# Optimization experiments

Hardware: AMD Instinct MI355X
Metric: run time of the kernel (lower is better)

The kernel has to match this reference:

```python
import jax, jax.numpy as jnp
import numpy as np

W0 = 30.0  # Sine frequency


def _bilinear_sample(plane, gx, gy):
    """torch.grid_sample(mode='bilinear', padding_mode='zeros', align_corners=True).
    plane: (C,H,W); gx,gy: (P,) normalized coords in [-1,1]. Returns (P,C)."""
    C, H, W = plane.shape
    ix = (gx + 1.0) * 0.5 * (W - 1)
    iy = (gy + 1.0) * 0.5 * (H - 1)
    x0 = jnp.floor(ix); y0 = jnp.floor(iy)
    x1 = x0 + 1.0;      y1 = y0 + 1.0
    wx1 = ix - x0; wx0 = 1.0 - wx1
    wy1 = iy - y0; wy0 = 1.0 - wy1

    def corner(xc, yc, w):
        valid = ((xc >= 0) & (xc <= W - 1) & (yc >= 0) & (yc <= H - 1)).astype(plane.dtype)
        xi = jnp.clip(xc, 0, W - 1).astype(jnp.int32)
        yi = jnp.clip(yc, 0, H - 1).astype(jnp.int32)
        return plane[:, yi, xi] * (w * valid)  # (C,P)

    out = (corner(x0, y0, wx0 * wy0) + corner(x1, y0, wx1 * wy0)
           + corner(x0, y1, wx0 * wy1) + corner(x1, y1, wx1 * wy1))
    return out.T  # (P,C)


def setup_inputs() -> dict:
    key = jax.random.key(0)
    ks = jax.random.split(key, 8)
    N = 500_000
    C, H, W = 128, 256, 256
    coords = jax.random.uniform(ks[0], (1, N, 3), jnp.float32, minval=-1.0, maxval=1.0)
    planes = [jax.random.normal(ks[1 + i], (1, C, H, W), jnp.float32) * 0.1 for i in range(3)]
    # Linear weights: first layer sine init, then frequency_init(30) for layers 2,3
    W1 = jax.random.uniform(ks[4], (C, C), jnp.float32, minval=-1.0 / C, maxval=1.0 / C)
    lim = np.sqrt(6.0 / C) / W0
    W2 = jax.random.uniform(ks[5], (C, C), jnp.float32, minval=-lim, maxval=lim)
    W3 = jax.random.uniform(ks[6], (1, C), jnp.float32, minval=-lim, maxval=lim)
    return {
        "coordinates": coords,
        "plane_xy": planes[0], "plane_yz": planes[1], "plane_xz": planes[2],
        "W1": W1, "b1": jnp.zeros((C,), jnp.float32),
        "W2": W2, "b2": jnp.zeros((C,), jnp.float32),
        "W3": W3, "b3": jnp.zeros((1,), jnp.float32),
    }


def reference(coordinates, plane_xy, plane_yz, plane_xz, W1, b1, W2, b2, W3, b3):
    B, N, _ = coordinates.shape  # B must be 1 (plane batch is 1, as in torch)
    c = coordinates.reshape(-1, 3)
    p0 = plane_xy[0]
    # NOTE: original module samples the *xz* coords from embeddings[0] (plane_xy) —
    # a bug we faithfully preserve — and multiplies [xy, xz, xz]; yz_embed is unused.
    xy = _bilinear_sample(p0, c[:, 0], c[:, 1])  # (P,C)
    xz = _bilinear_sample(p0, c[:, 0], c[:, 2])  # (P,C)
    features = xy * xz * xz
    h = jnp.sin(W0 * (features @ W1.T + b1))
    h = jnp.sin(W0 * (h @ W2.T + b2))
    out = h @ W3.T + b3
    return out.reshape(B, N, 1)
```

## Files before the change

kernel.cpp:

```cpp
#include <hip/hip_runtime.h>
#include <hip/hip_fp16.h>

typedef float f32x4 __attribute__((ext_vector_type(4)));
typedef _Float16 f16x8 __attribute__((ext_vector_type(8)));

#define CDIM 128
#define HW 256
#define NBINS 256
#define BINCAP 2560
#define TILES_PER_BIN 10
#define BINS_PER_XCD 32
#define GRID_MAIN 256

#define LDS_FENCE() asm volatile("" ::: "memory")

__global__ __launch_bounds__(256) void k_transpose(const float* __restrict__ plane,
                                                   unsigned short* __restrict__ planeT) {
    __shared__ unsigned short tile[32][130];
    int tid = threadIdx.x;
    int y  = blockIdx.x >> 3;
    int x0 = (blockIdx.x & 7) * 32;
    int tx = tid & 31, tc = tid >> 5;
    for (int cc = 0; cc < 128; cc += 8) {
        int c = cc + tc;
        float v = plane[c * (HW * HW) + y * HW + x0 + tx];
        tile[tx][c] = __half_as_ushort(__float2half(v));
    }
    __syncthreads();
    for (int it = 0; it < 16; ++it) {
        int idx = it * 256 + tid;
        int c = idx & 127, xi = idx >> 7;
        planeT[(y * HW + x0 + xi) * CDIM + c] = tile[xi][c];
    }
}

__global__ __launch_bounds__(256) void k_wconv(const float* __restrict__ W1,
                                               const float* __restrict__ W2,
                                               unsigned short* __restrict__ W1h,
                                               unsigned short* __restrict__ W2h) {
    int i = blockIdx.x * 256 + threadIdx.x;
    if (i < 16384) W1h[i] = __half_as_ushort(__float2half(W1[i]));
    else           W2h[i - 16384] = __half_as_ushort(__float2half(W2[i - 16384]));
}

__global__ __launch_bounds__(256) void k_scatter(const float* __restrict__ coords,
                                                 float4* __restrict__ bins,
                                                 int* __restrict__ cursor, int N) {
    __shared__ int hist[NBINS];
    __shared__ int rnk[NBINS];
    __shared__ int base[NBINS];
    const int tid = threadIdx.x;
    hist[tid] = 0; rnk[tid] = 0;
    __syncthreads();

    const int start = blockIdx.x * 2048;
    float gx[8], gy[8], gz[8]; int bn[8];
#pragma unroll
    for (int k = 0; k < 8; ++k) {
        int p = start + k * 256 + tid;
        if (p < N) {
            gx[k] = coords[p * 3 + 0];
            gy[k] = coords[p * 3 + 1];
            gz[k] = coords[p * 3 + 2];
            float ix = (gx[k] + 1.f) * 127.5f;
            bn[k] = max(0, min((int)floorf(ix), HW - 1));
            atomicAdd(&hist[bn[k]], 1);
        } else bn[k] = -1;
    }
    __syncthreads();
    if (hist[tid] > 0) base[tid] = atomicAdd(&cursor[tid], hist[tid]);
    __syncthreads();
#pragma unroll
    for (int k = 0; k < 8; ++k) {
        if (bn[k] >= 0) {
            int p = start + k * 256 + tid;
            int r = atomicAdd(&rnk[bn[k]], 1);
            int pos = base[bn[k]] + r;
            if (pos < BINCAP) {
                float4 rec; rec.x = gx[k]; rec.y = gy[k]; rec.z = gz[k];
                rec.w = __int_as_float(p);
                bins[(size_t)bn[k] * BINCAP + pos] = rec;
            }
        }
    }
}

struct PrepT {
    int off[8];
    __half2 w[4];
    __half2 v[4];
};

__device__ __forceinline__ PrepT prepV(float gx, float gy, float gz, int cg) {
    PrepT r;
    float ix = (gx + 1.f) * 127.5f;
    float iy = (gy + 1.f) * 127.5f;
    float iz = (gz + 1.f) * 127.5f;
    float xf = floorf(ix), yf = floorf(iy), zf = floorf(iz);
    float wx1 = ix - xf, wy1 = iy - yf, wz1 = iz - zf;
    float wx0 = 1.f - wx1, wy0 = 1.f - wy1, wz0 = 1.f - wz1;
    int x0 = max(0, min((int)xf, HW - 1));
    int y0 = max(0, min((int)yf, HW - 1));
    int z0 = max(0, min((int)zf, HW - 1));
    int x1 = min(x0 + 1, HW - 1);
    int y1 = min(y0 + 1, HW - 1);
    int z1 = min(z0 + 1, HW - 1);
    int cx0 = x0 * CDIM + cg * 8, cx1 = x1 * CDIM + cg * 8;
    r.off[0] = (y0 << 15) + cx0; r.off[1] = (y0 << 15) + cx1;
    r.off[2] = (y1 << 15) + cx0; r.off[3] = (y1 << 15) + cx1;
    r.off[4] = (z0 << 15) + cx0; r.off[5] = (z0 << 15) + cx1;
    r.off[6] = (z1 << 15) + cx0; r.off[7] = (z1 << 15) + cx1;
    r.w[0] = __float2half2_rn(wy0 * wx0);
    r.w[1] = __float2half2_rn(wy0 * wx1);
    r.w[2] = __float2half2_rn(wy1 * wx0);
    r.w[3] = __float2half2_rn(wy1 * wx1);
    r.v[0] = __float2half2_rn(wz0 * wx0);
    r.v[1] = __float2half2_rn(wz0 * wx1);
    r.v[2] = __float2half2_rn(wz1 * wx0);
    r.v[3] = __float2half2_rn(wz1 * wx1);
    return r;
}

struct LdT { uint4 d[8]; };

__device__ __forceinline__ LdT ld8(const unsigned short* __restrict__ planeT, const PrepT& a) {
    LdT r;
#pragma unroll
    for (int c = 0; c < 8; ++c)
        r.d[c] = *reinterpret_cast<const uint4*>(planeT + a.off[c]);
    return r;
}

__device__ __forceinline__ __half2 geth2(const uint4& u, int g) {
    const unsigned* p = reinterpret_cast<const unsigned*>(&u);
    return __builtin_bit_cast(__half2, p[g]);
}

__device__ __forceinline__ void interp_store(unsigned short* dst, const PrepT& a, const LdT& L) {
    unsigned o[4];
#pragma unroll
    for (int g = 0; g < 4; ++g) {
        __half2 xy = __hmul2(a.w[0], geth2(L.d[0], g));
        xy = __hfma2(a.w[1], geth2(L.d[1], g), xy);
        xy = __hfma2(a.w[2], geth2(L.d[2], g), xy);
        xy = __hfma2(a.w[3], geth2(L.d[3], g), xy);
        __half2 xz = __hmul2(a.v[0], geth2(L.d[4], g));
        xz = __hfma2(a.v[1], geth2(L.d[5], g), xz);
        xz = __hfma2(a.v[2], geth2(L.d[6], g), xz);
        xz = __hfma2(a.v[3], geth2(L.d[7], g), xz);
        __half2 f = __hmul2(xy, __hmul2(xz, xz));
        o[g] = __builtin_bit_cast(unsigned, f);
    }
    uint4 pack; pack.x = o[0]; pack.y = o[1]; pack.z = o[2]; pack.w = o[3];
    *reinterpret_cast<uint4*>(dst) = pack;
}

template <bool SORTED>
__global__ __launch_bounds__(512, 2) void k_all(const float* __restrict__ coords,
                                                const float4* __restrict__ bins,
                                                const int* __restrict__ cursor,
                                                const unsigned short* __restrict__ planeT,
                                                const unsigned short* __restrict__ W1h,
                                                const unsigned short* __restrict__ W2h,
                                                const float* __restrict__ b1,
                                                const float* __restrict__ b2,
                                                const float* __restrict__ W3,
                                                const float* __restrict__ b3,
                                                float* __restrict__ out, int N) {
    __shared__ alignas(16) uint4 W1L[128][16];
    __shared__ alignas(16) uint4 W2L[128][16];
    __shared__ alignas(16) unsigned short featS[256][128];

    const int tid  = threadIdx.x;
    const int wave = tid >> 6, lane = tid & 63;
    const int ro2  = wave * 32;
    const int j = lane & 15, rg = lane >> 4;
    const int pt = lane >> 4, cg = lane & 15;

#pragma unroll
    for (int i = 0; i < 4; ++i) {
        int idx = i * 512 + tid;
        int row = idx >> 4, col = idx & 15;
        W1L[row][col ^ (row & 15)] = reinterpret_cast<const uint4*>(W1h)[idx];
        W2L[row][col ^ (row & 15)] = reinterpret_cast<const uint4*>(W2h)[idx];
    }
    float b1v[8], b2v[8], w3v[8];
#pragma unroll
    for (int nt = 0; nt < 8; ++nt) {
        b1v[nt] = 30.f * b1[nt * 16 + j];
        b2v[nt] = 30.f * b2[nt * 16 + j];
        w3v[nt] = W3[nt * 16 + j];
    }
    const float bb3 = b3[0];
    __syncthreads();

    const int ntt = SORTED ? (NBINS * TILES_PER_BIN) : ((N + 255) >> 8);
    for (int tt = blockIdx.x; tt < ntt; tt += gridDim.x) {
        int bin = 0, base = 0, cnt = 0, pbase = 0;
        if (SORTED) {
            int xcd = tt & 7, jj = tt >> 3;
            bin  = xcd * BINS_PER_XCD + jj / TILES_PER_BIN;
            base = (jj % TILES_PER_BIN) * 256;
            cnt  = min(cursor[bin], BINCAP);
            if (base >= cnt) continue;
        } else {
            pbase = tt * 256 + ro2;
        }
        const float4* brec = bins + (size_t)bin * BINCAP;

#pragma unroll
        for (int grp = 0; grp < 2; ++grp) {
            PrepT a0, a1, a2, a3;
#pragma unroll
            for (int it = 0; it < 4; ++it) {
                int pl = grp * 16 + it * 4 + pt;
                float gx, gy, gz;
                if (SORTED) {
                    int q = min(base + ro2 + pl, cnt - 1);
                    float4 s = brec[q];
                    gx = s.x; gy = s.y; gz = s.z;
                } else {
                    int p = min(pbase + pl, N - 1);
                    gx = coords[p * 3 + 0];
                    gy = coords[p * 3 + 1];
                    gz = coords[p * 3 + 2];
                }
                PrepT a = prepV(gx, gy, gz, cg);
                if (it == 0) a0 = a; else if (it == 1) a1 = a;
                else if (it == 2) a2 = a; else a3 = a;
            }
            LdT d0 = ld8(planeT, a0);
            LdT d1 = ld8(planeT, a1);
            LdT d2 = ld8(planeT, a2);
            LdT d3 = ld8(planeT, a3);
            int r0 = grp * 16 + 0 * 4 + pt;
            int r1 = grp * 16 + 1 * 4 + pt;
            int r2 = grp * 16 + 2 * 4 + pt;
            int r3 = grp * 16 + 3 * 4 + pt;
            interp_store(&featS[ro2 + r0][(cg ^ (r0 & 15)) * 8], a0, d0);
            interp_store(&featS[ro2 + r1][(cg ^ (r1 & 15)) * 8], a1, d1);
            interp_store(&featS[ro2 + r2][(cg ^ (r2 & 15)) * 8], a2, d2);
            interp_store(&featS[ro2 + r3][(cg ^ (r3 & 15)) * 8], a3, d3);
        }

        LDS_FENCE();

        f32x4 acc[2][8];
#pragma unroll
        for (int g = 0; g < 2; ++g)
#pragma unroll
            for (int nt = 0; nt < 8; ++nt) acc[g][nt] = (f32x4){0.f, 0.f, 0.f, 0.f};

        f16x8 af[2][4];
#pragma unroll
        for (int g = 0; g < 2; ++g)
#pragma unroll
            for (int kk = 0; kk < 4; ++kk)
                af[g][kk] = __builtin_bit_cast(f16x8, *reinterpret_cast<const uint4*>(
                    &featS[ro2 + g * 16 + j][((kk * 4 + rg) ^ j) * 8]));

#pragma unroll
        for (int kk = 0; kk < 4; ++kk) {
            f16x8 bf[8];
#pragma unroll
            for (int nt = 0; nt < 8; ++nt)
                bf[nt] = __builtin_bit_cast(f16x8, W1L[nt * 16 + j][(kk * 4 + rg) ^ j]);
#pragma unroll
            for (int nt = 0; nt < 8; ++nt) {
                acc[0][nt] = __builtin_amdgcn_mfma_f32_16x16x32_f16(af[0][kk], bf[nt], acc[0][nt], 0, 0, 0);
                acc[1][nt] = __builtin_amdgcn_mfma_f32_16x16x32_f16(af[1][kk], bf[nt], acc[1][nt], 0, 0, 0);
            }
        }

        LDS_FENCE();

#pragma unroll
        for (int g = 0; g < 2; ++g)
#pragma unroll
            for (int nt = 0; nt < 8; ++nt) {
#pragma unroll
                for (int r = 0; r < 4; ++r) {
                    float h = __sinf(fmaf(30.f, acc[g][nt][r], b1v[nt]));
                    int row15 = rg * 4 + r;
                    int gc = (nt * 2 + (j >> 3)) ^ row15;
                    featS[ro2 + g * 16 + row15][gc * 8 + (j & 7)] = __half_as_ushort(__float2half(h));
                }
            }

        LDS_FENCE();

        f32x4 acc2[2][8];
#pragma unroll
        for (int g = 0; g < 2; ++g)
#pragma unroll
            for (int nt = 0; nt < 8; ++nt) acc2[g][nt] = (f32x4){0.f, 0.f, 0.f, 0.f};

        f16x8 af2[2][4];
#pragma unroll
        for (int g = 0; g < 2; ++g)
#pragma unroll
            for (int kk = 0; kk < 4; ++kk)
                af2[g][kk] = __builtin_bit_cast(f16x8, *reinterpret_cast<const uint4*>(
                    &featS[ro2 + g * 16 + j][((kk * 4 + rg) ^ j) * 8]));

#pragma unroll
        for (int kk = 0; kk < 4; ++kk) {
            f16x8 bf[8];
#pragma unroll
            for (int nt = 0; nt < 8; ++nt)
                bf[nt] = __builtin_bit_cast(f16x8, W2L[nt * 16 + j][(kk * 4 + rg) ^ j]);
#pragma unroll
            for (int nt = 0; nt < 8; ++nt) {
                acc2[0][nt] = __builtin_amdgcn_mfma_f32_16x16x32_f16(af2[0][kk], bf[nt], acc2[0][nt], 0, 0, 0);
                acc2[1][nt] = __builtin_amdgcn_mfma_f32_16x16x32_f16(af2[1][kk], bf[nt], acc2[1][nt], 0, 0, 0);
            }
        }

#pragma unroll
        for (int g = 0; g < 2; ++g) {
            float part[4] = {0.f, 0.f, 0.f, 0.f};
#pragma unroll
            for (int nt = 0; nt < 8; ++nt) {
#pragma unroll
                for (int r = 0; r < 4; ++r)
                    part[r] += __sinf(fmaf(30.f, acc2[g][nt][r], b2v[nt])) * w3v[nt];
            }
#pragma unroll
            for (int off = 1; off < 16; off <<= 1) {
#pragma unroll
                for (int r = 0; r < 4; ++r) part[r] += __shfl_xor(part[r], off, 64);
            }
            if (j == 0) {
#pragma unroll
                for (int r = 0; r < 4; ++r) {
                    int pl = g * 16 + rg * 4 + r;
                    if (SORTED) {
                        int q = base + ro2 + pl;
                        if (q < cnt) {
                            int orig = __float_as_int(brec[q].w);
                            out[orig] = part[r] + bb3;
                        }
                    } else {
                        int p = pbase + pl;
                        if (p < N) out[p] = part[r] + bb3;
                    }
                }
            }
        }

        LDS_FENCE();
    }
}

extern "C" void kernel_launch(void* const* d_in, const int* in_sizes, int n_in,
                              void* d_out, int out_size, void* d_ws, size_t ws_size,
                              hipStream_t stream) {
    const float* coords = (const float*)d_in[0];
    const float* plane  = (const float*)d_in[1];
    const float* W1     = (const float*)d_in[4];
    const float* b1     = (const float*)d_in[5];
    const float* W2     = (const float*)d_in[6];
    const float* b2     = (const float*)d_in[7];
    const float* W3     = (const float*)d_in[8];
    const float* b3     = (const float*)d_in[9];
    float* out = (float*)d_out;
    int N = in_sizes[0] / 3;

    char* ws = (char*)d_ws;
    unsigned short* planeT = (unsigned short*)ws;
    unsigned short* W1h = (unsigned short*)(ws + 16777216);
    unsigned short* W2h = (unsigned short*)(ws + 16809984);
    int*    cursor = (int*)(ws + 16842752);
    float4* bins   = (float4*)(ws + 16843776);
    const size_t need = 16843776 + (size_t)NBINS * BINCAP * 16;

    k_transpose<<<dim3(HW * 8), dim3(256), 0, stream>>>(plane, planeT);
    k_wconv<<<dim3(128), dim3(256), 0, stream>>>(W1, W2, W1h, W2h);

    if (ws_size >= need) {
        hipMemsetAsync(cursor, 0, NBINS * sizeof(int), stream);
        k_scatter<<<dim3((N + 2047) / 2048), dim3(256), 0, stream>>>(coords, bins, cursor, N);
        k_all<true><<<dim3(GRID_MAIN), dim3(512), 0, stream>>>(
            coords, bins, cursor, planeT, W1h, W2h, b1, b2, W3, b3, out, N);
    } else {
        k_all<false><<<dim3(GRID_MAIN), dim3(512), 0, stream>>>(
            coords, bins, cursor, planeT, W1h, W2h, b1, b2, W3, b3, out, N);
    }
}
```

Baseline: 116.4 us.

## Gather sampled features directly into MFMA A-fragment registers, skipping LDS staging

```diff
diff --git a/kernel.cpp b/kernel.cpp
--- a/kernel.cpp
+++ b/kernel.cpp
@@ -91,7 +91,7 @@
     __half2 v[4];
 };
 
-__device__ __forceinline__ PrepT prepV(float gx, float gy, float gz, int cg) {
+__device__ __forceinline__ PrepT prepV(float gx, float gy, float gz) {
     PrepT r;
     float ix = (gx + 1.f) * 127.5f;
     float iy = (gy + 1.f) * 127.5f;
@@ -105,7 +105,7 @@
     int x1 = min(x0 + 1, HW - 1);
     int y1 = min(y0 + 1, HW - 1);
     int z1 = min(z0 + 1, HW - 1);
-    int cx0 = x0 * CDIM + cg * 8, cx1 = x1 * CDIM + cg * 8;
+    int cx0 = x0 * CDIM, cx1 = x1 * CDIM;
     r.off[0] = (y0 << 15) + cx0; r.off[1] = (y0 << 15) + cx1;
     r.off[2] = (y1 << 15) + cx0; r.off[3] = (y1 << 15) + cx1;
     r.off[4] = (z0 << 15) + cx0; r.off[5] = (z0 << 15) + cx1;
@@ -123,11 +123,13 @@
 
 struct LdT { uint4 d[8]; };
 
-__device__ __forceinline__ LdT ld8(const unsigned short* __restrict__ planeT, const PrepT& a) {
+__device__ __forceinline__ LdT ld8g(const unsigned short* __restrict__ planeT,
+                                    const PrepT& a, int g) {
     LdT r;
+    const int go = g * 8;
 #pragma unroll
     for (int c = 0; c < 8; ++c)
-        r.d[c] = *reinterpret_cast<const uint4*>(planeT + a.off[c]);
+        r.d[c] = *reinterpret_cast<const uint4*>(planeT + a.off[c] + go);
     return r;
 }
 
@@ -136,7 +138,7 @@
     return __builtin_bit_cast(__half2, p[g]);
 }
 
-__device__ __forceinline__ void interp_store(unsigned short* dst, const PrepT& a, const LdT& L) {
+__device__ __forceinline__ uint4 interpR(const PrepT& a, const LdT& L) {
     unsigned o[4];
 #pragma unroll
     for (int g = 0; g < 4; ++g) {
@@ -152,7 +154,7 @@
         o[g] = __builtin_bit_cast(unsigned, f);
     }
     uint4 pack; pack.x = o[0]; pack.y = o[1]; pack.z = o[2]; pack.w = o[3];
-    *reinterpret_cast<uint4*>(dst) = pack;
+    return pack;
 }
 
 template <bool SORTED>
@@ -175,7 +177,6 @@
     const int wave = tid >> 6, lane = tid & 63;
     const int ro2  = wave * 32;
     const int j = lane & 15, rg = lane >> 4;
-    const int pt = lane >> 4, cg = lane & 15;
 
 #pragma unroll
     for (int i = 0; i < 4; ++i) {
@@ -208,56 +209,36 @@
         }
         const float4* brec = bins + (size_t)bin * BINCAP;
 
-#pragma unroll
-        for (int grp = 0; grp < 2; ++grp) {
-            PrepT a0, a1, a2, a3;
-#pragma unroll
-            for (int it = 0; it < 4; ++it) {
-                int pl = grp * 16 + it * 4 + pt;
-                float gx, gy, gz;
-                if (SORTED) {
-                    int q = min(base + ro2 + pl, cnt - 1);
-                    float4 s = brec[q];
-                    gx = s.x; gy = s.y; gz = s.z;
-                } else {
-                    int p = min(pbase + pl, N - 1);
-                    gx = coords[p * 3 + 0];
-                    gy = coords[p * 3 + 1];
-                    gz = coords[p * 3 + 2];
-                }
-                PrepT a = prepV(gx, gy, gz, cg);
-                if (it == 0) a0 = a; else if (it == 1) a1 = a;
-                else if (it == 2) a2 = a; else a3 = a;
-            }
-            LdT d0 = ld8(planeT, a0);
-            LdT d1 = ld8(planeT, a1);
-            LdT d2 = ld8(planeT, a2);
-            LdT d3 = ld8(planeT, a3);
-            int r0 = grp * 16 + 0 * 4 + pt;
-            int r1 = grp * 16 + 1 * 4 + pt;
-            int r2 = grp * 16 + 2 * 4 + pt;
-            int r3 = grp * 16 + 3 * 4 + pt;
-            interp_store(&featS[ro2 + r0][(cg ^ (r0 & 15)) * 8], a0, d0);
-            interp_store(&featS[ro2 + r1][(cg ^ (r1 & 15)) * 8], a1, d1);
-            interp_store(&featS[ro2 + r2][(cg ^ (r2 & 15)) * 8], a2, d2);
-            interp_store(&featS[ro2 + r3][(cg ^ (r3 & 15)) * 8], a3, d3);
-        }
-
-        LDS_FENCE();
+        f16x8 af[2][4];
+#pragma unroll
+        for (int g2 = 0; g2 < 2; ++g2) {
+            float gx, gy, gz;
+            if (SORTED) {
+                int q = min(base + ro2 + g2 * 16 + j, cnt - 1);
+                float4 s = brec[q];
+                gx = s.x; gy = s.y; gz = s.z;
+            } else {
+                int p = min(pbase + g2 * 16 + j, N - 1);
+                gx = coords[p * 3 + 0];
+                gy = coords[p * 3 + 1];
+                gz = coords[p * 3 + 2];
+            }
+            PrepT a = prepV(gx, gy, gz);
+            LdT d0 = ld8g(planeT, a, 0 * 4 + rg);
+            LdT d1 = ld8g(planeT, a, 1 * 4 + rg);
+            af[g2][0] = __builtin_bit_cast(f16x8, interpR(a, d0));
+            d0 = ld8g(planeT, a, 2 * 4 + rg);
+            af[g2][1] = __builtin_bit_cast(f16x8, interpR(a, d1));
+            d1 = ld8g(planeT, a, 3 * 4 + rg);
+            af[g2][2] = __builtin_bit_cast(f16x8, interpR(a, d0));
+            af[g2][3] = __builtin_bit_cast(f16x8, interpR(a, d1));
+        }
 
         f32x4 acc[2][8];
 #pragma unroll
         for (int g = 0; g < 2; ++g)
 #pragma unroll
             for (int nt = 0; nt < 8; ++nt) acc[g][nt] = (f32x4){0.f, 0.f, 0.f, 0.f};
-
-        f16x8 af[2][4];
-#pragma unroll
-        for (int g = 0; g < 2; ++g)
-#pragma unroll
-            for (int kk = 0; kk < 4; ++kk)
-                af[g][kk] = __builtin_bit_cast(f16x8, *reinterpret_cast<const uint4*>(
-                    &featS[ro2 + g * 16 + j][((kk * 4 + rg) ^ j) * 8]));
 
 #pragma unroll
         for (int kk = 0; kk < 4; ++kk) {
@@ -271,8 +252,6 @@
                 acc[1][nt] = __builtin_amdgcn_mfma_f32_16x16x32_f16(af[1][kk], bf[nt], acc[1][nt], 0, 0, 0);
             }
         }
-
-        LDS_FENCE();
 
 #pragma unroll
         for (int g = 0; g < 2; ++g)
```

Result: slower. 169.1 us (+45.2%).
